# Optimization experiments

Measured on AMD Instinct MI355X. Metric: run time of the kernel, lower is better.

## Reference

```python
import jax, jax.numpy as jnp
import numpy as np

EPS = 1e-9


def _squash(s, axis=-1):
    # squash(s) = (|s|^2 / (1+|s|^2)) * s / |s|
    sq = jnp.sum(jnp.square(s), axis=axis, keepdims=True)
    norm = jnp.sqrt(sq + EPS)
    return (sq / (1.0 + sq)) * (s / norm)


def setup_inputs() -> dict:
    key = jax.random.key(0)
    B, N_IN, N_OUT, ATOMS = 32, 2048, 64, 16
    votes = jax.random.normal(key, (B, N_IN, N_OUT, ATOMS), dtype=jnp.float32)
    return {"votes": votes, "num_routing": 3}


def reference(votes, num_routing):
    # votes: [B, in_caps, out_caps, atoms]
    temper = 1.0
    softmax_in = False
    B, n_in, n_out, atoms = votes.shape
    logits = jnp.zeros((B, n_in, n_out, 1), dtype=votes.dtype)
    pose = None
    for i in range(num_routing):
        # coupling coefficients: softmax over out-caps axis (softmax_in=False)
        ax = 1 if softmax_in else 2
        c = jax.nn.softmax(logits * temper, axis=ax)  # [B, in, out, 1]
        # weighted pooling over input capsules -> [B, 1, out, atoms]
        preact = jnp.sum(c * votes, axis=1, keepdims=True)
        pose = _squash(preact, axis=-1)
        if i < num_routing - 1:
            # agreement: <votes, pose> over atoms -> [B, in, out, 1]
            logits = logits + jnp.sum(votes * pose, axis=-1, keepdims=True)
    prob = jnp.sqrt(jnp.sum(jnp.square(pose), axis=-1, keepdims=True) + EPS)  # [B,1,out,1]
    pose_out = jnp.squeeze(pose, axis=-3)          # [B, out, atoms]
    prob_out = jnp.squeeze(prob, axis=(-3, -1))    # [B, out]
    return pose_out, prob_out
```

## Files before the change

kernel.cpp:

```cpp
#include <hip/hip_runtime.h>


#define NB 32
#define NIN 2048
#define NOUT 64
#define ATOMS 16
#define EPSF 1e-9f

#define ROWS_PER_WAVE 32
#define WAVES_PER_BLOCK 4
#define ROWS_PER_BLOCK (ROWS_PER_WAVE * WAVES_PER_BLOCK)
#define CHUNKS (NIN / ROWS_PER_BLOCK)

template <int USE_POSE>
__global__ __launch_bounds__(256) void route_pass(
    const float* __restrict__ votes,
    const float* __restrict__ pose_accum,
    float* __restrict__ preact)
{
    const int b    = blockIdx.x / CHUNKS;
    const int chunk = blockIdx.x % CHUNKS;
    const int wave = threadIdx.x >> 6;
    const int lane = threadIdx.x & 63;

    float pose[ATOMS];
    if (USE_POSE) {
        const float4* p4 = reinterpret_cast<const float4*>(pose_accum) + (b * NOUT + lane) * 4;
        float4 q0 = p4[0], q1 = p4[1], q2 = p4[2], q3 = p4[3];
        pose[0]=q0.x; pose[1]=q0.y; pose[2]=q0.z; pose[3]=q0.w;
        pose[4]=q1.x; pose[5]=q1.y; pose[6]=q1.z; pose[7]=q1.w;
        pose[8]=q2.x; pose[9]=q2.y; pose[10]=q2.z; pose[11]=q2.w;
        pose[12]=q3.x; pose[13]=q3.y; pose[14]=q3.z; pose[15]=q3.w;
    }

    float acc[ATOMS];
#pragma unroll
    for (int a = 0; a < ATOMS; ++a) acc[a] = 0.0f;

    const int in0 = chunk * ROWS_PER_BLOCK + wave * ROWS_PER_WAVE;
    const float4* vrow = reinterpret_cast<const float4*>(votes)
                       + ((size_t)(b * NIN + in0) * NOUT + lane) * (ATOMS / 4);

#pragma unroll 2
    for (int r = 0; r < ROWS_PER_WAVE; ++r) {
        const float4* vp = vrow + (size_t)r * (NOUT * (ATOMS / 4));
        float4 c0 = vp[0], c1 = vp[1], c2 = vp[2], c3 = vp[3];
        float v[ATOMS];
        v[0]=c0.x; v[1]=c0.y; v[2]=c0.z; v[3]=c0.w;
        v[4]=c1.x; v[5]=c1.y; v[6]=c1.z; v[7]=c1.w;
        v[8]=c2.x; v[9]=c2.y; v[10]=c2.z; v[11]=c2.w;
        v[12]=c3.x; v[13]=c3.y; v[14]=c3.z; v[15]=c3.w;

        float cc;
        if (USE_POSE) {
            float logit = 0.0f;
#pragma unroll
            for (int a = 0; a < ATOMS; ++a) logit = fmaf(v[a], pose[a], logit);
            float m = logit;
#pragma unroll
            for (int mask = 32; mask >= 1; mask >>= 1)
                m = fmaxf(m, __shfl_xor(m, mask, 64));
            float e = __expf(logit - m);
            float s = e;
#pragma unroll
            for (int mask = 32; mask >= 1; mask >>= 1)
                s += __shfl_xor(s, mask, 64);
            cc = e / s;
        } else {
            cc = 1.0f / 64.0f;
        }
#pragma unroll
        for (int a = 0; a < ATOMS; ++a) acc[a] = fmaf(cc, v[a], acc[a]);
    }

    __shared__ float red[WAVES_PER_BLOCK * NOUT * ATOMS];
#pragma unroll
    for (int a = 0; a < ATOMS; ++a)
        red[(wave * NOUT + lane) * ATOMS + a] = acc[a];
    __syncthreads();

    for (int idx = threadIdx.x; idx < NOUT * ATOMS; idx += 256) {
        float t = red[idx] + red[NOUT * ATOMS + idx]
                + red[2 * NOUT * ATOMS + idx] + red[3 * NOUT * ATOMS + idx];
        atomicAdd(&preact[b * NOUT * ATOMS + idx], t);
    }
}

__global__ __launch_bounds__(256) void squash_k(
    const float* __restrict__ preact,
    float* __restrict__ pose_accum,
    float* __restrict__ d_out,
    int mode)
{
    int idx = blockIdx.x * 256 + threadIdx.x;
    float s = preact[idx];
    float sq = s * s;
#pragma unroll
    for (int mask = 1; mask < ATOMS; mask <<= 1)
        sq += __shfl_xor(sq, mask, 64);
    float norm = sqrtf(sq + EPSF);
    float f = (sq / (1.0f + sq)) / norm;
    float p = f * s;
    if (mode == 0) {
        pose_accum[idx] = p;
    } else if (mode == 1) {
        pose_accum[idx] += p;
    } else {
        d_out[idx] = p;
        if ((idx & (ATOMS - 1)) == 0) {
            float psq = f * f * sq;
            d_out[NB * NOUT * ATOMS + (idx >> 4)] = sqrtf(psq + EPSF);
        }
    }
}

extern "C" void kernel_launch(void* const* d_in, const int* in_sizes, int n_in,
                              void* d_out, int out_size, void* d_ws, size_t ws_size,
                              hipStream_t stream) {
    const float* votes = (const float*)d_in[0];
    float* out = (float*)d_out;

    float* preact     = (float*)d_ws;
    float* pose_accum = preact + NB * NOUT * ATOMS;
    const size_t pre_bytes = (size_t)NB * NOUT * ATOMS * sizeof(float);

    dim3 blk(256);
    dim3 grid_route(NB * CHUNKS);
    dim3 grid_sq(NB * NOUT * ATOMS / 256);

    hipMemsetAsync(preact, 0, pre_bytes, stream);
    route_pass<0><<<grid_route, blk, 0, stream>>>(votes, nullptr, preact);
    squash_k<<<grid_sq, blk, 0, stream>>>(preact, pose_accum, nullptr, 0);

    hipMemsetAsync(preact, 0, pre_bytes, stream);
    route_pass<1><<<grid_route, blk, 0, stream>>>(votes, pose_accum, preact);
    squash_k<<<grid_sq, blk, 0, stream>>>(preact, pose_accum, nullptr, 1);

    hipMemsetAsync(preact, 0, pre_bytes, stream);
    route_pass<1><<<grid_route, blk, 0, stream>>>(votes, pose_accum, preact);
    squash_k<<<grid_sq, blk, 0, stream>>>(preact, nullptr, out, 2);
}
```

Before: 458.0 us.

## Batch row loads and shuffles in routing pass, fold preact clearing into squash

The routing kernel now loads four vote rows at once and interleaves their softmax shuffle reductions, so more memory requests and cross-lane operations are in flight per wave. Each wave handles fewer rows (8 instead of 32), which gives four times as many blocks, and a minimum occupancy hint is added. The softmax max-subtraction reduction is dropped on the assumption that logits stay small enough for exp not to overflow. The two middle memsets are replaced by having squash_k zero preact after reading it. The trade-offs are more atomicAdd traffic into preact, a numerical-safety risk if logits grow large, and aliased restrict pointers in squash_k.

```diff
diff --git a/kernel.cpp b/kernel.cpp
--- a/kernel.cpp
+++ b/kernel.cpp
@@ -7,21 +7,22 @@
 #define ATOMS 16
 #define EPSF 1e-9f
 
-#define ROWS_PER_WAVE 32
+#define ROWS_PER_WAVE 8
 #define WAVES_PER_BLOCK 4
 #define ROWS_PER_BLOCK (ROWS_PER_WAVE * WAVES_PER_BLOCK)
 #define CHUNKS (NIN / ROWS_PER_BLOCK)
+#define RBATCH 4
 
 template <int USE_POSE>
-__global__ __launch_bounds__(256) void route_pass(
+__global__ __launch_bounds__(256, 4) void route_pass(
     const float* __restrict__ votes,
     const float* __restrict__ pose_accum,
     float* __restrict__ preact)
 {
-    const int b    = blockIdx.x / CHUNKS;
+    const int b     = blockIdx.x / CHUNKS;
     const int chunk = blockIdx.x % CHUNKS;
-    const int wave = threadIdx.x >> 6;
-    const int lane = threadIdx.x & 63;
+    const int wave  = threadIdx.x >> 6;
+    const int lane  = threadIdx.x & 63;
 
     float pose[ATOMS];
     if (USE_POSE) {
@@ -41,36 +42,44 @@
     const float4* vrow = reinterpret_cast<const float4*>(votes)
                        + ((size_t)(b * NIN + in0) * NOUT + lane) * (ATOMS / 4);
 
-#pragma unroll 2
-    for (int r = 0; r < ROWS_PER_WAVE; ++r) {
-        const float4* vp = vrow + (size_t)r * (NOUT * (ATOMS / 4));
-        float4 c0 = vp[0], c1 = vp[1], c2 = vp[2], c3 = vp[3];
-        float v[ATOMS];
-        v[0]=c0.x; v[1]=c0.y; v[2]=c0.z; v[3]=c0.w;
-        v[4]=c1.x; v[5]=c1.y; v[6]=c1.z; v[7]=c1.w;
-        v[8]=c2.x; v[9]=c2.y; v[10]=c2.z; v[11]=c2.w;
-        v[12]=c3.x; v[13]=c3.y; v[14]=c3.z; v[15]=c3.w;
+    for (int r0 = 0; r0 < ROWS_PER_WAVE; r0 += RBATCH) {
+        float4 c[RBATCH][4];
+#pragma unroll
+        for (int r = 0; r < RBATCH; ++r) {
+            const float4* vp = vrow + (size_t)(r0 + r) * (NOUT * (ATOMS / 4));
+            c[r][0] = vp[0]; c[r][1] = vp[1]; c[r][2] = vp[2]; c[r][3] = vp[3];
+        }
 
-        float cc;
+        float cc[RBATCH];
         if (USE_POSE) {
-            float logit = 0.0f;
+            float s[RBATCH], e[RBATCH];
 #pragma unroll
-            for (int a = 0; a < ATOMS; ++a) logit = fmaf(v[a], pose[a], logit);
-            float m = logit;
+            for (int r = 0; r < RBATCH; ++r) {
+                const float* v = reinterpret_cast<const float*>(&c[r][0]);
+                float logit = 0.0f;
 #pragma unroll
-            for (int mask = 32; mask >= 1; mask >>= 1)
-                m = fmaxf(m, __shfl_xor(m, mask, 64));
-            float e = __expf(logit - m);
-            float s = e;
+                for (int a = 0; a < ATOMS; ++a) logit = fmaf(v[a], pose[a], logit);
+                e[r] = __expf(logit);
+                s[r] = e[r];
+            }
 #pragma unroll
-            for (int mask = 32; mask >= 1; mask >>= 1)
-                s += __shfl_xor(s, mask, 64);
-            cc = e / s;
+            for (int mask = 32; mask >= 1; mask >>= 1) {
+#pragma unroll
+                for (int r = 0; r < RBATCH; ++r)
+                    s[r] += __shfl_xor(s[r], mask, 64);
+            }
+#pragma unroll
+            for (int r = 0; r < RBATCH; ++r) cc[r] = e[r] / s[r];
         } else {
-            cc = 1.0f / 64.0f;
+#pragma unroll
+            for (int r = 0; r < RBATCH; ++r) cc[r] = 1.0f / 64.0f;
         }
 #pragma unroll
-        for (int a = 0; a < ATOMS; ++a) acc[a] = fmaf(cc, v[a], acc[a]);
+        for (int r = 0; r < RBATCH; ++r) {
+            const float* v = reinterpret_cast<const float*>(&c[r][0]);
+#pragma unroll
+            for (int a = 0; a < ATOMS; ++a) acc[a] = fmaf(cc[r], v[a], acc[a]);
+        }
     }
 
     __shared__ float red[WAVES_PER_BLOCK * NOUT * ATOMS];
@@ -87,13 +96,14 @@
 }
 
 __global__ __launch_bounds__(256) void squash_k(
-    const float* __restrict__ preact,
+    const float* __restrict__ preact_in,
+    float* __restrict__ preact_clr,
     float* __restrict__ pose_accum,
     float* __restrict__ d_out,
     int mode)
 {
     int idx = blockIdx.x * 256 + threadIdx.x;
-    float s = preact[idx];
+    float s = preact_in[idx];
     float sq = s * s;
 #pragma unroll
     for (int mask = 1; mask < ATOMS; mask <<= 1)
@@ -103,8 +113,10 @@
     float p = f * s;
     if (mode == 0) {
         pose_accum[idx] = p;
+        preact_clr[idx] = 0.0f;
     } else if (mode == 1) {
         pose_accum[idx] += p;
+        preact_clr[idx] = 0.0f;
     } else {
         d_out[idx] = p;
         if ((idx & (ATOMS - 1)) == 0) {
@@ -129,14 +141,13 @@
     dim3 grid_sq(NB * NOUT * ATOMS / 256);
 
     hipMemsetAsync(preact, 0, pre_bytes, stream);
+
     route_pass<0><<<grid_route, blk, 0, stream>>>(votes, nullptr, preact);
-    squash_k<<<grid_sq, blk, 0, stream>>>(preact, pose_accum, nullptr, 0);
+    squash_k<<<grid_sq, blk, 0, stream>>>(preact, preact, pose_accum, nullptr, 0);
 
-    hipMemsetAsync(preact, 0, pre_bytes, stream);
     route_pass<1><<<grid_route, blk, 0, stream>>>(votes, pose_accum, preact);
-    squash_k<<<grid_sq, blk, 0, stream>>>(preact, pose_accum, nullptr, 1);
+    squash_k<<<grid_sq, blk, 0, stream>>>(preact, preact, pose_accum, nullptr, 1);
 
-    hipMemsetAsync(preact, 0, pre_bytes, stream);
     route_pass<1><<<grid_route, blk, 0, stream>>>(votes, pose_accum, preact);
-    squash_k<<<grid_sq, blk, 0, stream>>>(preact, nullptr, out, 2);
+    squash_k<<<grid_sq, blk, 0, stream>>>(preact, nullptr, nullptr, out, 2);
 }
```

Result: no change. 458.3 us (+0.1%).
